# Kernel tuning notes

Measured on AMD Instinct MI355X. Metric: run time of the kernel, lower is better.

## Reference

```python
import jax, jax.numpy as jnp
import numpy as np

EMB = 1024
HEADS = 16
HEAD_DIM = EMB // HEADS


def setup_inputs() -> dict:
    key = jax.random.key(0)
    ks = jax.random.split(key, 11)
    B, S = 2, 2048
    scale = 1.0 / np.sqrt(EMB)
    inp = {
        "query": jax.random.normal(ks[0], (B, S, EMB), jnp.float32),
        "key": jax.random.normal(ks[1], (B, S, EMB), jnp.float32),
        "value": jax.random.normal(ks[2], (B, S, EMB), jnp.float32),
        "Wq": jax.random.normal(ks[3], (EMB, EMB), jnp.float32) * scale,
        "bq": jnp.zeros((EMB,), jnp.float32),
        "Wk": jax.random.normal(ks[4], (EMB, EMB), jnp.float32) * scale,
        "bk": jnp.zeros((EMB,), jnp.float32),
        "Wv": jax.random.normal(ks[5], (EMB, EMB), jnp.float32) * scale,
        "bv": jnp.zeros((EMB,), jnp.float32),
        "Wo": jax.random.normal(ks[6], (EMB, EMB), jnp.float32) * scale,
        "bo": jnp.zeros((EMB,), jnp.float32),
    }
    return inp


def reference(query, key, value, Wq, bq, Wk, bk, Wv, bv, Wo, bo):
    B, S, _ = query.shape
    # Linear projections (torch Linear: x @ W.T + b)
    Q = query @ Wq.T + bq
    K = key @ Wk.T + bk
    V = value @ Wv.T + bv
    # [B, H, S, Dh]
    Q = Q.reshape(B, S, HEADS, HEAD_DIM).transpose(0, 2, 1, 3)
    K = K.reshape(B, S, HEADS, HEAD_DIM).transpose(0, 2, 1, 3)
    V = V.reshape(B, S, HEADS, HEAD_DIM).transpose(0, 2, 1, 3)
    scores = jnp.einsum("bhqd,bhkd->bhqk", Q, K) / jnp.sqrt(
        jnp.asarray(HEAD_DIM, Q.dtype)
    )
    attn = jax.nn.softmax(scores, axis=-1)
    ctx = jnp.einsum("bhqk,bhkd->bhqd", attn, V)
    ctx = ctx.transpose(0, 2, 1, 3).reshape(B, S, EMB)
    return ctx @ Wo.T + bo
```

## Files before the change

kernel.cpp:

```cpp
#include <hip/hip_runtime.h>
#include <stdint.h>

typedef __attribute__((ext_vector_type(8)))  __bf16 bf16x8;
typedef __attribute__((ext_vector_type(4)))  float  f32x4;
typedef __attribute__((ext_vector_type(16))) float  f32x16;
typedef __attribute__((ext_vector_type(8)))  ushort u16x8;
typedef __attribute__((ext_vector_type(4)))  ushort u16x4;
typedef __attribute__((ext_vector_type(4)))  uint   u32x4;

#define LOG2E 1.44269504088896f

__device__ __forceinline__ ushort f2bf(float f) {
  uint32_t u = __float_as_uint(f);
  u += 0x7fffu + ((u >> 16) & 1u);
  return (ushort)(u >> 16);
}
__device__ __forceinline__ float bf2f(ushort h) {
  return __uint_as_float(((uint32_t)h) << 16);
}
__device__ __forceinline__ void gload16(const void* g, void* l) {
  __builtin_amdgcn_global_load_lds((const __attribute__((address_space(1))) void*)g,
                                   (__attribute__((address_space(3))) void*)l, 16, 0, 0);
}
__device__ __forceinline__ f32x4 mfma16(bf16x8 a, bf16x8 b, f32x4 c) {
  return __builtin_amdgcn_mfma_f32_16x16x32_bf16(a, b, c, 0, 0, 0);
}
__device__ __forceinline__ f32x16 mfma32(bf16x8 a, bf16x8 b, f32x16 c) {
  return __builtin_amdgcn_mfma_f32_32x32x16_bf16(a, b, c, 0, 0, 0);
}
__device__ __forceinline__ int swz(int row, int byteoff) {
  return row * 128 + (byteoff ^ ((row & 7) << 4));
}
__device__ __forceinline__ uint cvtpk(float lo, float hi) {
  uint w;
  asm("v_cvt_pk_bf16_f32 %0, %1, %2" : "=v"(w) : "v"(lo), "v"(hi));
  return w;
}
__device__ __forceinline__ void plswap(uint& a, uint& b) {
  asm("v_permlane32_swap_b32 %0, %1" : "+v"(a), "+v"(b));
}

struct CvtArgs { const float* src[7]; ushort* dst[7]; };

__global__ __launch_bounds__(256) void cvt_all(CvtArgs a) {
  const int bid = blockIdx.x;
  int seg, base;
  if (bid < 2048) { seg = bid >> 9;              base = bid & 511; }
  else            { seg = 4 + ((bid - 2048) >> 11); base = (bid - 2048) & 2047; }
  const int i = base * 256 + threadIdx.x;
  const f32x4* s = (const f32x4*)a.src[seg];
  f32x4 x = s[2 * i], y = s[2 * i + 1];
  u16x8 o;
  o[0] = f2bf(x[0]); o[1] = f2bf(x[1]); o[2] = f2bf(x[2]); o[3] = f2bf(x[3]);
  o[4] = f2bf(y[0]); o[5] = f2bf(y[1]); o[6] = f2bf(y[2]); o[7] = f2bf(y[3]);
  ((u16x8*)a.dst[seg])[i] = o;
}

struct QKVArgs {
  const ushort* A0; const ushort* A1; const ushort* A2;
  const ushort* W0; const ushort* W1; const ushort* W2;
  const float* b0; const float* b1; const float* b2;
  ushort* Qo; ushort* Ko; ushort* Vo;
};

__global__ __launch_bounds__(256) void qkv_gemm(QKVArgs args) {
  __shared__ ushort Ash[128 * 32];
  __shared__ ushort Bsh[128 * 32];

  const int z = blockIdx.z;
  const ushort* Ab   = z == 0 ? args.A0 : (z == 1 ? args.A1 : args.A2);
  const ushort* Wb   = z == 0 ? args.W0 : (z == 1 ? args.W1 : args.W2);
  const float*  bias = z == 0 ? args.b0 : (z == 1 ? args.b1 : args.b2);

  const int tid = threadIdx.x;
  const int lane = tid & 63, wid = tid >> 6;
  const int l15 = lane & 15, g = lane >> 4;
  const int wr = wid >> 1, wc = wid & 1;
  const int tm = blockIdx.x * 128, tn = blockIdx.y * 128;

  const f32x4 fz = {0.f, 0.f, 0.f, 0.f};
  f32x4 acc[4][4];
#pragma unroll
  for (int m = 0; m < 4; ++m)
#pragma unroll
    for (int n = 0; n < 4; ++n) acc[m][n] = fz;

  for (int kt = 0; kt < 1024; kt += 32) {
#pragma unroll
    for (int c = 0; c < 2; ++c) {
      const int chunk = wid * 2 + c;
      const int off = chunk * 1024 + lane * 16;
      const int row = off >> 6;
      const int ke = (off & 63) >> 1;
      gload16(Wb + (size_t)(tn + row) * 1024 + kt + ke, &Bsh[chunk * 512]);
      gload16(Ab + (size_t)(tm + row) * 1024 + kt + ke, &Ash[chunk * 512]);
    }
    __syncthreads();

    bf16x8 af[4], bfr[4];
#pragma unroll
    for (int m = 0; m < 4; ++m)
      af[m] = *(const bf16x8*)&Ash[(wr * 64 + m * 16 + l15) * 32 + g * 8];
#pragma unroll
    for (int n = 0; n < 4; ++n)
      bfr[n] = *(const bf16x8*)&Bsh[(wc * 64 + n * 16 + l15) * 32 + g * 8];
#pragma unroll
    for (int m = 0; m < 4; ++m)
#pragma unroll
      for (int n = 0; n < 4; ++n) acc[m][n] = mfma16(af[m], bfr[n], acc[m][n]);
    __syncthreads();
  }

#pragma unroll
  for (int n = 0; n < 4; ++n) {
    const int col = tn + wc * 64 + n * 16 + l15;
    const float bv = bias[col];
    const int h = col >> 6, d = col & 63;
#pragma unroll
    for (int m = 0; m < 4; ++m) {
      const int row0 = tm + wr * 64 + m * 16 + g * 4;
      if (z == 2) {
        const int b = row0 >> 11, s0 = row0 & 2047;
        u16x4 pk;
#pragma unroll
        for (int r = 0; r < 4; ++r) pk[r] = f2bf(acc[m][n][r] + bv);
        *(u16x4*)&args.Vo[((size_t)((b * 16 + h) * 64 + d)) * 2048 + s0] = pk;
      } else {
        ushort* O = z ? args.Ko : args.Qo;
#pragma unroll
        for (int r = 0; r < 4; ++r) {
          const int row = row0 + r;
          const int b = row >> 11, s = row & 2047;
          O[((size_t)(b * 16 + h) * 2048 + s) * 64 + d] = f2bf(acc[m][n][r] + bv);
        }
      }
    }
  }
}

__global__ __launch_bounds__(256) void attn_fwd(const ushort* __restrict__ Qb,
                                                const ushort* __restrict__ Kb,
                                                const ushort* __restrict__ VTb,
                                                ushort* __restrict__ ctxb) {
  __shared__ char Ksh[64 * 128];
  __shared__ char Vsh[64 * 128];
  __shared__ float Ssc[4][32];

  const int tid = threadIdx.x;
  const int lane = tid & 63, wid = tid >> 6;
  const int l31 = lane & 31, hi = lane >> 5;
  const int bh = blockIdx.y;
  const int q0 = blockIdx.x * 128 + wid * 32;

  const ushort* Qh = Qb + (size_t)bh * 2048 * 64;
  const ushort* Kh = Kb + (size_t)bh * 2048 * 64;
  const ushort* Vh = VTb + (size_t)bh * 64 * 2048;

  bf16x8 qf[4];
  {
    const ushort* qrow = Qh + (size_t)(q0 + l31) * 64;
#pragma unroll
    for (int dt = 0; dt < 4; ++dt) {
      u16x8 raw = *(const u16x8*)&qrow[dt * 16 + hi * 8];
      u16x8 sc;
#pragma unroll
      for (int j = 0; j < 8; ++j) sc[j] = f2bf(bf2f(raw[j]) * 0.125f);
      qf[dt] = __builtin_bit_cast(bf16x8, sc);
    }
  }

  f32x16 o0 = {}, o1 = {};
  float m = -1e30f, lsum = 0.f;

  const int si = tid >> 2, sc4i = tid & 3;
  const ushort* kg = &Kh[(size_t)si * 64 + sc4i * 16];
  const ushort* vg = &Vh[(size_t)si * 2048 + sc4i * 16];

  u16x8 kr0, kr1, vr0, vr1;
  kr0 = *(const u16x8*)kg;  kr1 = *(const u16x8*)(kg + 8);
  vr0 = *(const u16x8*)vg;  vr1 = *(const u16x8*)(vg + 8);
  *(u16x8*)(Ksh + swz(si, sc4i * 32))      = kr0;
  *(u16x8*)(Ksh + swz(si, sc4i * 32 + 16)) = kr1;
  *(u16x8*)(Vsh + swz(si, sc4i * 32))      = vr0;
  *(u16x8*)(Vsh + swz(si, sc4i * 32 + 16)) = vr1;
  __syncthreads();

  for (int t = 0; t < 32; ++t) {
    if (t + 1 < 32) {
      const int kt2 = (t + 1) * 64;
      kr0 = *(const u16x8*)(kg + (size_t)kt2 * 64);
      kr1 = *(const u16x8*)(kg + (size_t)kt2 * 64 + 8);
      vr0 = *(const u16x8*)(vg + kt2);
      vr1 = *(const u16x8*)(vg + kt2 + 8);
    }

    f32x16 P0 = {}, P1 = {};
    __builtin_amdgcn_s_setprio(1);
#pragma unroll
    for (int dt = 0; dt < 4; ++dt) {
      bf16x8 kf0 = *(const bf16x8*)(Ksh + swz(l31,      dt * 32 + hi * 16));
      bf16x8 kf1 = *(const bf16x8*)(Ksh + swz(32 + l31, dt * 32 + hi * 16));
      P0 = mfma32(kf0, qf[dt], P0);
      P1 = mfma32(kf1, qf[dt], P1);
    }
    __builtin_amdgcn_s_setprio(0);

    float pm = fmaxf(P0[0], P1[0]);
#pragma unroll
    for (int r = 1; r + 1 < 16; r += 2) {
      pm = fmaxf(fmaxf(pm, P0[r]), P0[r + 1]);
      pm = fmaxf(fmaxf(pm, P1[r]), P1[r + 1]);
    }
    pm = fmaxf(fmaxf(pm, P0[15]), P1[15]);
    pm = fmaxf(pm, __shfl_xor(pm, 32));

    if (!__all(pm <= m + 8.f)) {
      const float mn = fmaxf(m, pm);
      const float scl = __builtin_amdgcn_exp2f((m - mn) * LOG2E);
      m = mn;
      lsum *= scl;
      Ssc[wid][l31] = scl;
      f32x4 s0 = *(const f32x4*)&Ssc[wid][hi * 4];
      f32x4 s1 = *(const f32x4*)&Ssc[wid][8 + hi * 4];
      f32x4 s2 = *(const f32x4*)&Ssc[wid][16 + hi * 4];
      f32x4 s3 = *(const f32x4*)&Ssc[wid][24 + hi * 4];
#pragma unroll
      for (int r = 0; r < 16; ++r) {
        const float sv = (r < 4 ? s0[r & 3] : r < 8 ? s1[r & 3] : r < 12 ? s2[r & 3] : s3[r & 3]);
        o0[r] *= sv; o1[r] *= sv;
      }
    }

    const float nml = -m * LOG2E;
#pragma unroll
    for (int r = 0; r < 16; ++r)
      P0[r] = __builtin_amdgcn_exp2f(__builtin_fmaf(P0[r], LOG2E, nml));
#pragma unroll
    for (int r = 0; r < 16; ++r)
      P1[r] = __builtin_amdgcn_exp2f(__builtin_fmaf(P1[r], LOG2E, nml));

    float rs = 0.f;
#pragma unroll
    for (int r = 0; r < 16; ++r) rs += P0[r] + P1[r];
    rs += __shfl_xor(rs, 32);
    lsum += rs;

    bf16x8 pa[4];
#pragma unroll
    for (int s = 0; s < 2; ++s) {
      const f32x16& P = s ? P1 : P0;
      uint a0 = cvtpk(P[0], P[1]),  b0 = cvtpk(P[4], P[5]);
      uint a1 = cvtpk(P[2], P[3]),  b1 = cvtpk(P[6], P[7]);
      plswap(a0, b0); plswap(a1, b1);
      pa[2 * s] = __builtin_bit_cast(bf16x8, (u32x4){a0, a1, b0, b1});
      uint a2 = cvtpk(P[8], P[9]),   b2 = cvtpk(P[12], P[13]);
      uint a3 = cvtpk(P[10], P[11]), b3 = cvtpk(P[14], P[15]);
      plswap(a2, b2); plswap(a3, b3);
      pa[2 * s + 1] = __builtin_bit_cast(bf16x8, (u32x4){a2, a3, b2, b3});
    }

    __builtin_amdgcn_s_setprio(1);
#pragma unroll
    for (int kk = 0; kk < 4; ++kk) {
      bf16x8 v0f = *(const bf16x8*)(Vsh + swz(l31,      kk * 32 + hi * 16));
      bf16x8 v1f = *(const bf16x8*)(Vsh + swz(32 + l31, kk * 32 + hi * 16));
      o0 = mfma32(pa[kk], v0f, o0);
      o1 = mfma32(pa[kk], v1f, o1);
    }
    __builtin_amdgcn_s_setprio(0);

    if (t + 1 < 32) {
      __syncthreads();
      *(u16x8*)(Ksh + swz(si, sc4i * 32))      = kr0;
      *(u16x8*)(Ksh + swz(si, sc4i * 32 + 16)) = kr1;
      *(u16x8*)(Vsh + swz(si, sc4i * 32))      = vr0;
      *(u16x8*)(Vsh + swz(si, sc4i * 32 + 16)) = vr1;
      __syncthreads();
    }
  }

  Ssc[wid][l31] = 1.0f / lsum;
  f32x4 i0 = *(const f32x4*)&Ssc[wid][hi * 4];
  f32x4 i1 = *(const f32x4*)&Ssc[wid][8 + hi * 4];
  f32x4 i2 = *(const f32x4*)&Ssc[wid][16 + hi * 4];
  f32x4 i3 = *(const f32x4*)&Ssc[wid][24 + hi * 4];
  const int b = bh >> 4, h = bh & 15;
#pragma unroll
  for (int r = 0; r < 16; ++r) {
    const float inv = (r < 4 ? i0[r & 3] : r < 8 ? i1[r & 3] : r < 12 ? i2[r & 3] : i3[r & 3]);
    const int q = q0 + (r & 3) + 8 * (r >> 2) + 4 * hi;
    const size_t base = ((size_t)(b * 2048 + q)) * 1024 + h * 64;
    ctxb[base + l31]      = f2bf(o0[r] * inv);
    ctxb[base + 32 + l31] = f2bf(o1[r] * inv);
  }
}

__global__ __launch_bounds__(256) void out_gemm(const ushort* __restrict__ A16,
                                                const ushort* __restrict__ Wb,
                                                const float* __restrict__ bias,
                                                float* __restrict__ O) {
  __shared__ ushort Ash[64 * 32];
  __shared__ ushort Bsh[128 * 32];

  const int tid = threadIdx.x;
  const int lane = tid & 63, wid = tid >> 6;
  const int l15 = lane & 15, g = lane >> 4;
  const int wr = wid >> 1, wc = wid & 1;
  const int tm = blockIdx.x * 64, tn = blockIdx.y * 128;

  const f32x4 fz = {0.f, 0.f, 0.f, 0.f};
  f32x4 acc[2][4];
#pragma unroll
  for (int m = 0; m < 2; ++m)
#pragma unroll
    for (int n = 0; n < 4; ++n) acc[m][n] = fz;

  for (int kt = 0; kt < 1024; kt += 32) {
#pragma unroll
    for (int c = 0; c < 2; ++c) {
      const int chunk = wid * 2 + c;
      const int off = chunk * 1024 + lane * 16;
      const int row = off >> 6;
      const int ke = (off & 63) >> 1;
      gload16(Wb + (size_t)(tn + row) * 1024 + kt + ke, &Bsh[chunk * 512]);
    }
    {
      const int off = wid * 1024 + lane * 16;
      const int row = off >> 6;
      const int ke = (off & 63) >> 1;
      gload16(A16 + (size_t)(tm + row) * 1024 + kt + ke, &Ash[wid * 512]);
    }
    __syncthreads();

    bf16x8 af[2], bfr[4];
#pragma unroll
    for (int m = 0; m < 2; ++m)
      af[m] = *(const bf16x8*)&Ash[(wr * 32 + m * 16 + l15) * 32 + g * 8];
#pragma unroll
    for (int n = 0; n < 4; ++n)
      bfr[n] = *(const bf16x8*)&Bsh[(wc * 64 + n * 16 + l15) * 32 + g * 8];
#pragma unroll
    for (int m = 0; m < 2; ++m)
#pragma unroll
      for (int n = 0; n < 4; ++n) acc[m][n] = mfma16(af[m], bfr[n], acc[m][n]);
    __syncthreads();
  }

#pragma unroll
  for (int n = 0; n < 4; ++n) {
    const int col = tn + wc * 64 + n * 16 + l15;
    const float bv = bias[col];
#pragma unroll
    for (int m = 0; m < 2; ++m) {
      const int row0 = tm + wr * 32 + m * 16 + g * 4;
#pragma unroll
      for (int r = 0; r < 4; ++r)
        O[(size_t)(row0 + r) * 1024 + col] = acc[m][n][r] + bv;
    }
  }
}

extern "C" void kernel_launch(void* const* d_in, const int* in_sizes, int n_in,
                              void* d_out, int out_size, void* d_ws, size_t ws_size,
                              hipStream_t stream) {
  const float* query = (const float*)d_in[0];
  const float* key_  = (const float*)d_in[1];
  const float* value = (const float*)d_in[2];
  const float* Wq = (const float*)d_in[3];
  const float* bq = (const float*)d_in[4];
  const float* Wk = (const float*)d_in[5];
  const float* bk = (const float*)d_in[6];
  const float* Wv = (const float*)d_in[7];
  const float* bv = (const float*)d_in[8];
  const float* Wo = (const float*)d_in[9];
  const float* bo = (const float*)d_in[10];

  ushort* ws = (ushort*)d_ws;
  ushort* Wqb = ws;
  ushort* Wkb = ws + (1u << 20);
  ushort* Wvb = ws + (2u << 20);
  ushort* Wob = ws + (3u << 20);
  ushort* Qb  = ws + (4u << 20);
  ushort* Kb  = Qb + (4u << 20);
  ushort* VTb = Kb + (4u << 20);
  ushort* ctx = VTb + (4u << 20);
  ushort* Xqb = ctx;
  ushort* Xkb = (ushort*)d_out;
  ushort* Xvb = (ushort*)d_out + (4u << 20);

  dim3 blk(256);

  CvtArgs ca;
  ca.src[0] = Wq;    ca.dst[0] = Wqb;
  ca.src[1] = Wk;    ca.dst[1] = Wkb;
  ca.src[2] = Wv;    ca.dst[2] = Wvb;
  ca.src[3] = Wo;    ca.dst[3] = Wob;
  ca.src[4] = query; ca.dst[4] = Xqb;
  ca.src[5] = key_;  ca.dst[5] = Xkb;
  ca.src[6] = value; ca.dst[6] = Xvb;
  cvt_all<<<8192, blk, 0, stream>>>(ca);

  QKVArgs a;
  a.A0 = Xqb;  a.A1 = Xkb;  a.A2 = Xvb;
  a.W0 = Wqb;  a.W1 = Wkb;  a.W2 = Wvb;
  a.b0 = bq;   a.b1 = bk;   a.b2 = bv;
  a.Qo = Qb;   a.Ko = Kb;   a.Vo = VTb;
  qkv_gemm<<<dim3(32, 8, 3), blk, 0, stream>>>(a);

  attn_fwd<<<dim3(16, 32), blk, 0, stream>>>(Qb, Kb, VTb, ctx);

  out_gemm<<<dim3(64, 8), blk, 0, stream>>>(ctx, Wob, bo, (float*)d_out);
}
```

Measured before the change: 140.6 us.

## Split attention over key halves and merge partials in a combine kernel

The attention kernel now processes half of the keys per block, with a third grid dimension selecting which half, doubling the number of blocks. Each block writes unnormalized bf16 partial outputs and its running max and sum. A new combine kernel merges the two halves with log-sum-exp weights. This aims to raise GPU occupancy for the attention stage, at the cost of an extra launch, extra memory traffic for the partials, and an additional bf16 rounding of the unnormalized output.

Result: slower. 147.8 us (+5.1%).

```diff
diff --git a/kernel.cpp b/kernel.cpp
--- a/kernel.cpp
+++ b/kernel.cpp
@@ -141,7 +141,8 @@
 __global__ __launch_bounds__(256) void attn_fwd(const ushort* __restrict__ Qb,
                                                 const ushort* __restrict__ Kb,
                                                 const ushort* __restrict__ VTb,
-                                                ushort* __restrict__ ctxb) {
+                                                ushort* __restrict__ Op,
+                                                float2* __restrict__ Ml) {
   __shared__ char Ksh[64 * 128];
   __shared__ char Vsh[64 * 128];
   __shared__ float Ssc[4][32];
@@ -150,6 +151,8 @@
   const int lane = tid & 63, wid = tid >> 6;
   const int l31 = lane & 31, hi = lane >> 5;
   const int bh = blockIdx.y;
+  const int zz = blockIdx.z;
+  const int kbase = zz * 1024;
   const int q0 = blockIdx.x * 128 + wid * 32;
 
   const ushort* Qh = Qb + (size_t)bh * 2048 * 64;
@@ -173,8 +176,8 @@
   float m = -1e30f, lsum = 0.f;
 
   const int si = tid >> 2, sc4i = tid & 3;
-  const ushort* kg = &Kh[(size_t)si * 64 + sc4i * 16];
-  const ushort* vg = &Vh[(size_t)si * 2048 + sc4i * 16];
+  const ushort* kg = &Kh[(size_t)(kbase + si) * 64 + sc4i * 16];
+  const ushort* vg = &Vh[(size_t)si * 2048 + kbase + sc4i * 16];
 
   u16x8 kr0, kr1, vr0, vr1;
   kr0 = *(const u16x8*)kg;  kr1 = *(const u16x8*)(kg + 8);
@@ -185,8 +188,8 @@
   *(u16x8*)(Vsh + swz(si, sc4i * 32 + 16)) = vr1;
   __syncthreads();
 
-  for (int t = 0; t < 32; ++t) {
-    if (t + 1 < 32) {
+  for (int t = 0; t < 16; ++t) {
+    if (t + 1 < 16) {
       const int kt2 = (t + 1) * 64;
       kr0 = *(const u16x8*)(kg + (size_t)kt2 * 64);
       kr1 = *(const u16x8*)(kg + (size_t)kt2 * 64 + 8);
@@ -269,7 +272,7 @@
     }
     __builtin_amdgcn_s_setprio(0);
 
-    if (t + 1 < 32) {
+    if (t + 1 < 16) {
       __syncthreads();
       *(u16x8*)(Ksh + swz(si, sc4i * 32))      = kr0;
       *(u16x8*)(Ksh + swz(si, sc4i * 32 + 16)) = kr1;
@@ -279,20 +282,44 @@
     }
   }
 
-  Ssc[wid][l31] = 1.0f / lsum;
-  f32x4 i0 = *(const f32x4*)&Ssc[wid][hi * 4];
-  f32x4 i1 = *(const f32x4*)&Ssc[wid][8 + hi * 4];
-  f32x4 i2 = *(const f32x4*)&Ssc[wid][16 + hi * 4];
-  f32x4 i3 = *(const f32x4*)&Ssc[wid][24 + hi * 4];
-  const int b = bh >> 4, h = bh & 15;
+  ushort* Ob = Op + ((size_t)(zz * 32 + bh) * 2048) * 64;
+  if (hi == 0)
+    Ml[(size_t)(zz * 32 + bh) * 2048 + q0 + l31] = make_float2(m, lsum);
 #pragma unroll
   for (int r = 0; r < 16; ++r) {
-    const float inv = (r < 4 ? i0[r & 3] : r < 8 ? i1[r & 3] : r < 12 ? i2[r & 3] : i3[r & 3]);
     const int q = q0 + (r & 3) + 8 * (r >> 2) + 4 * hi;
-    const size_t base = ((size_t)(b * 2048 + q)) * 1024 + h * 64;
-    ctxb[base + l31]      = f2bf(o0[r] * inv);
-    ctxb[base + 32 + l31] = f2bf(o1[r] * inv);
-  }
+    ushort* row = Ob + (size_t)q * 64;
+    row[l31]      = f2bf(o0[r]);
+    row[32 + l31] = f2bf(o1[r]);
+  }
+}
+
+__global__ __launch_bounds__(256) void attn_combine(const ushort* __restrict__ Op,
+                                                    const float2* __restrict__ Ml,
+                                                    ushort* __restrict__ ctxb) {
+  const int tid = blockIdx.x * 256 + threadIdx.x;
+  const size_t i8 = (size_t)tid * 8;
+  const int d  = (int)(i8 & 63);
+  const int h  = (int)((i8 >> 6) & 15);
+  const int s  = (int)((i8 >> 10) & 2047);
+  const int b  = (int)(i8 >> 21);
+  const size_t row = (size_t)(b * 16 + h) * 2048 + s;
+
+  const float2 ml0 = Ml[row];
+  const float2 ml1 = Ml[row + (size_t)32 * 2048];
+  const float M = fmaxf(ml0.x, ml1.x);
+  float w0 = __builtin_amdgcn_exp2f((ml0.x - M) * LOG2E);
+  float w1 = __builtin_amdgcn_exp2f((ml1.x - M) * LOG2E);
+  const float inv = 1.0f / (ml0.y * w0 + ml1.y * w1);
+  w0 *= inv; w1 *= inv;
+
+  u16x8 p0 = *(const u16x8*)&Op[row * 64 + d];
+  u16x8 p1 = *(const u16x8*)&Op[(row + (size_t)32 * 2048) * 64 + d];
+  u16x8 o;
+#pragma unroll
+  for (int j = 0; j < 8; ++j)
+    o[j] = f2bf(bf2f(p0[j]) * w0 + bf2f(p1[j]) * w1);
+  ((u16x8*)ctxb)[tid] = o;
 }
 
 __global__ __launch_bounds__(256) void out_gemm(const ushort* __restrict__ A16,
@@ -384,9 +411,11 @@
   ushort* Kb  = Qb + (4u << 20);
   ushort* VTb = Kb + (4u << 20);
   ushort* ctx = VTb + (4u << 20);
+  float2* Ml  = (float2*)(ws + (20u << 20));
   ushort* Xqb = ctx;
   ushort* Xkb = (ushort*)d_out;
   ushort* Xvb = (ushort*)d_out + (4u << 20);
+  ushort* Op  = (ushort*)d_out;
 
   dim3 blk(256);
 
@@ -407,7 +436,8 @@
   a.Qo = Qb;   a.Ko = Kb;   a.Vo = VTb;
   qkv_gemm<<<dim3(32, 8, 3), blk, 0, stream>>>(a);
 
-  attn_fwd<<<dim3(16, 32), blk, 0, stream>>>(Qb, Kb, VTb, ctx);
+  attn_fwd<<<dim3(16, 32, 2), blk, 0, stream>>>(Qb, Kb, VTb, Op, Ml);
+  attn_combine<<<2048, blk, 0, stream>>>(Op, Ml, ctx);
 
   out_gemm<<<dim3(64, 8), blk, 0, stream>>>(ctx, Wob, bo, (float*)d_out);
 }
```
